# Kernel optimization log

Hardware: AMD Instinct MI355X
Metric: run time of the kernel (lower is better)

Reference implementation:

```python
import jax, jax.numpy as jnp
import numpy as np

N_NODES = 100000
N_EDGES = 1600000
F_IN = 512
HEADS = 8
C1 = 8            # hidden per head in conv1
N_CLASSES = 40
NEG_SLOPE = 0.2
EPS = 1e-16


def setup_inputs() -> dict:
    key = jax.random.key(0)
    ks = jax.random.split(key, 12)
    x = jax.random.normal(ks[0], (N_NODES, F_IN), dtype=jnp.float32)
    # edges with src != dst (PyG SuperGAT removes then re-adds self-loops)
    src = jax.random.randint(ks[1], (N_EDGES,), 0, N_NODES)
    off = jax.random.randint(ks[2], (N_EDGES,), 1, N_NODES)
    dst = (src + off) % N_NODES
    edge_index = jnp.stack([src, dst]).astype(jnp.int64)
    def glorot(k, shape):
        fan = shape[0] + shape[-1]
        return jax.random.uniform(k, shape, jnp.float32, -1.0, 1.0) * np.sqrt(6.0 / fan)
    W1 = glorot(ks[3], (F_IN, HEADS * C1))
    att_l1 = glorot(ks[4], (HEADS, C1))
    att_r1 = glorot(ks[5], (HEADS, C1))
    b1 = jnp.zeros((HEADS * C1,), jnp.float32)
    W2 = glorot(ks[6], (HEADS * C1, HEADS * N_CLASSES))
    att_l2 = glorot(ks[7], (HEADS, N_CLASSES))
    att_r2 = glorot(ks[8], (HEADS, N_CLASSES))
    b2 = jnp.zeros((N_CLASSES,), jnp.float32)
    return {"x": x, "edge_index": edge_index, "W1": W1, "att_l1": att_l1,
            "att_r1": att_r1, "b1": b1, "W2": W2, "att_l2": att_l2,
            "att_r2": att_r2, "b2": b2}


def supergat_conv(x, edge_index, W, att_l, att_r, bias, concat):
    """SuperGATConv with attention_type='MX', eval mode (no dropout)."""
    N = x.shape[0]
    H, C = att_l.shape
    xw = (x @ W).reshape(N, H, C)
    loops = jnp.arange(N)
    src = jnp.concatenate([edge_index[0], loops])  # j (source)
    dst = jnp.concatenate([edge_index[1], loops])  # i (target)
    x_j = xw[src]                                   # [E,H,C]
    x_i = xw[dst]                                   # [E,H,C]
    # MX attention: GO score gated by sigmoid of DP logits
    logits = jnp.einsum('ehc,ehc->eh', x_i, x_j)
    alpha = jnp.einsum('ehc,hc->eh', x_j, att_l) + jnp.einsum('ehc,hc->eh', x_i, att_r)
    alpha = alpha * jax.nn.sigmoid(logits)
    alpha = jax.nn.leaky_relu(alpha, NEG_SLOPE)
    # segment softmax over incoming edges of each destination node
    amax = jax.ops.segment_max(alpha, dst, num_segments=N)
    e = jnp.exp(alpha - amax[dst])
    denom = jax.ops.segment_sum(e, dst, num_segments=N)
    a = e / (denom[dst] + EPS)
    out = jax.ops.segment_sum(x_j * a[..., None], dst, num_segments=N)  # [N,H,C]
    out = out.reshape(N, H * C) if concat else out.mean(axis=1)
    return out + bias


def reference(x, edge_index, W1, att_l1, att_r1, b1, W2, att_l2, att_r2, b2):
    # eval mode: F.dropout(p=0.6) is identity, att_loss is 0
    h = jax.nn.elu(supergat_conv(x, edge_index, W1, att_l1, att_r1, b1, concat=True))
    out = supergat_conv(h, edge_index, W2, att_l2, att_r2, b2, concat=False)
    att_loss = jnp.float32(0.0)
    return jax.nn.log_softmax(out, axis=-1), att_loss
```

## Files before the change

### kernel.cpp

```cpp
#include <hip/hip_runtime.h>
#include <cstdint>

#define N_NODES 100000
#define N_EDGES 1600000
#define SCAN_NB 196

typedef short bf16x8 __attribute__((ext_vector_type(8)));
typedef float f32x4 __attribute__((ext_vector_type(4)));
typedef float f32x2 __attribute__((ext_vector_type(2)));

__device__ __forceinline__ uint16_t f2bf(float f) {
    uint32_t b = __float_as_uint(f);
    return (uint16_t)((b + 0x7fffu + ((b >> 16) & 1u)) >> 16);
}
__device__ __forceinline__ float bfval(uint16_t u) {
    return __uint_as_float(((uint32_t)u) << 16);
}
__device__ __forceinline__ float blo(uint32_t u) { return __uint_as_float(u << 16); }
__device__ __forceinline__ float bhi(uint32_t u) { return __uint_as_float(u & 0xffff0000u); }

__device__ __forceinline__ float fast_rcp(float x) { return __builtin_amdgcn_rcpf(x); }
__device__ __forceinline__ float swz_xadd8(float x) {
    int s = __builtin_amdgcn_ds_swizzle(__float_as_int(x), 0x201F);
    return x + __int_as_float(s);
}
__device__ __forceinline__ float swz_xadd16(float x) {
    int s = __builtin_amdgcn_ds_swizzle(__float_as_int(x), 0x401F);
    return x + __int_as_float(s);
}

__global__ __launch_bounds__(512) void prep_k(const float* __restrict__ W1,
        const float* __restrict__ W2, const float* __restrict__ attl,
        const float* __restrict__ attr,
        uint16_t* __restrict__ w1hi, uint16_t* __restrict__ w1lo,
        float* __restrict__ wl2, float* __restrict__ wr2,
        uint16_t* __restrict__ w2z, uint16_t* __restrict__ mhi,
        uint16_t* __restrict__ mlo) {
    __shared__ float Wh[64 * 40];
    int b = blockIdx.x, tid = threadIdx.x;
    if (b < 8) {
        int gid = b * 512 + tid;
        int c = gid & 63, kg = gid >> 6;
        uint32_t dh[4], dl[4];
        #pragma unroll
        for (int t = 0; t < 4; ++t) {
            float v0 = W1[(kg * 8 + 2 * t) * 64 + c];
            float v1 = W1[(kg * 8 + 2 * t + 1) * 64 + c];
            uint16_t h0 = f2bf(v0), h1 = f2bf(v1);
            uint16_t l0 = f2bf(v0 - bfval(h0)), l1 = f2bf(v1 - bfval(h1));
            dh[t] = h0 | ((uint32_t)h1 << 16);
            dl[t] = l0 | ((uint32_t)l1 << 16);
        }
        *(uint4*)(w1hi + (long)c * 512 + kg * 8) = make_uint4(dh[0], dh[1], dh[2], dh[3]);
        *(uint4*)(w1lo + (long)c * 512 + kg * 8) = make_uint4(dl[0], dl[1], dl[2], dl[3]);
    } else if (b == 8) {
        int h = tid >> 6, k = tid & 63;
        float sl = 0.f, sr = 0.f;
        #pragma unroll 8
        for (int c = 0; c < 40; ++c) {
            float w = W2[k * 320 + h * 40 + c];
            sl += w * attl[h * 40 + c];
            sr += w * attr[h * 40 + c];
        }
        wl2[tid] = sl; wr2[tid] = sr;
    } else if (b < 57) {
        int t = (b - 9) * 512 + tid;
        int c = t >> 9, kap = t & 511;
        int h = kap >> 6, k = kap & 63;
        float v = (c < 40) ? W2[k * 320 + h * 40 + c] : 0.f;
        w2z[c * 512 + kap] = f2bf(v);
    } else {
        int h = b - 57;
        for (int t = tid; t < 2560; t += 512) {
            int k = t / 40, c = t % 40;
            Wh[k * 40 + c] = W2[k * 320 + h * 40 + c];
        }
        __syncthreads();
        #pragma unroll
        for (int r = 0; r < 8; ++r) {
            int o = r * 512 + tid;
            int kp = o >> 6, k = o & 63;
            float s = 0.f;
            #pragma unroll 8
            for (int c = 0; c < 40; ++c) s += Wh[k * 40 + c] * Wh[kp * 40 + c];
            uint16_t hi = f2bf(s);
            uint16_t lo = f2bf(s - bfval(hi));
            mhi[(h * 64 + kp) * 64 + k] = hi;
            mlo[(h * 64 + kp) * 64 + k] = lo;
        }
    }
}

__global__ __launch_bounds__(512) void gemm1_mfma(const float* __restrict__ x,
        const uint16_t* __restrict__ w1hi, const uint16_t* __restrict__ w1lo,
        float* __restrict__ xw1, uint16_t* __restrict__ xw1b) {
    __shared__ __align__(16) char Ah[128 * 144];
    __shared__ __align__(16) char Al[128 * 144];
    __shared__ __align__(16) char Bh[64 * 144];
    __shared__ __align__(16) char Bl[64 * 144];
    int tid = threadIdx.x;
    int l = tid & 63, w = tid >> 6;
    long base = (long)blockIdx.x * 128;
    f32x4 acc[4];
    #pragma unroll
    for (int ct = 0; ct < 4; ++ct)
        #pragma unroll
        for (int j = 0; j < 4; ++j) acc[ct][j] = 0.f;

    for (int kb = 0; kb < 512; kb += 64) {
        __syncthreads();
        #pragma unroll
        for (int it = 0; it < 2; ++it) {
            int idx = tid + it * 512;
            int row = idx >> 3, kc = idx & 7;
            long r = base + row; if (r >= N_NODES) r = N_NODES - 1;
            const float4* p = (const float4*)(x + r * 512 + kb + kc * 8);
            float4 f0 = p[0], f1 = p[1];
            float v[8] = {f0.x, f0.y, f0.z, f0.w, f1.x, f1.y, f1.z, f1.w};
            uint32_t dh[4], dl[4];
            #pragma unroll
            for (int t = 0; t < 4; ++t) {
                uint16_t h0 = f2bf(v[2 * t]),     h1 = f2bf(v[2 * t + 1]);
                uint16_t l0 = f2bf(v[2 * t] - bfval(h0));
                uint16_t l1 = f2bf(v[2 * t + 1] - bfval(h1));
                dh[t] = h0 | ((uint32_t)h1 << 16);
                dl[t] = l0 | ((uint32_t)l1 << 16);
            }
            *(uint4*)(Ah + row * 144 + kc * 16) = make_uint4(dh[0], dh[1], dh[2], dh[3]);
            *(uint4*)(Al + row * 144 + kc * 16) = make_uint4(dl[0], dl[1], dl[2], dl[3]);
        }
        {
            int c = tid >> 3, kc = tid & 7;
            *(uint4*)(Bh + c * 144 + kc * 16) =
                *(const uint4*)(w1hi + (long)c * 512 + kb + kc * 8);
            *(uint4*)(Bl + c * 144 + kc * 16) =
                *(const uint4*)(w1lo + (long)c * 512 + kb + kc * 8);
        }
        __syncthreads();
        #pragma unroll
        for (int kk = 0; kk < 2; ++kk) {
            int aoff = (w * 16 + (l & 15)) * 144 + kk * 64 + (l >> 4) * 16;
            bf16x8 ah = *(const bf16x8*)(Ah + aoff);
            bf16x8 alo = *(const bf16x8*)(Al + aoff);
            #pragma unroll
            for (int ct = 0; ct < 4; ++ct) {
                int boff = (ct * 16 + (l & 15)) * 144 + kk * 64 + (l >> 4) * 16;
                bf16x8 bh = *(const bf16x8*)(Bh + boff);
                bf16x8 bl = *(const bf16x8*)(Bl + boff);
                acc[ct] = __builtin_amdgcn_mfma_f32_16x16x32_bf16(ah, bh, acc[ct], 0, 0, 0);
                acc[ct] = __builtin_amdgcn_mfma_f32_16x16x32_bf16(alo, bh, acc[ct], 0, 0, 0);
                acc[ct] = __builtin_amdgcn_mfma_f32_16x16x32_bf16(ah, bl, acc[ct], 0, 0, 0);
            }
        }
    }
    int nrow = w * 16 + (l >> 4) * 4;
    #pragma unroll
    for (int ct = 0; ct < 4; ++ct)
        #pragma unroll
        for (int j = 0; j < 4; ++j) {
            long node = base + nrow + j;
            if (node < N_NODES) {
                int col = ct * 16 + (l & 15);
                xw1[node * 64 + col] = acc[ct][j];
                xw1b[node * 64 + col] = f2bf(acc[ct][j]);
            }
        }
}

__global__ __launch_bounds__(512) void ygemm_mfma(const uint16_t* __restrict__ hjb,
        const uint16_t* __restrict__ mhi, const uint16_t* __restrict__ mlo,
        uint16_t* __restrict__ Y16) {
    __shared__ __align__(16) char Bh[256 * 144];
    __shared__ __align__(16) char Bl[256 * 144];
    int tid = threadIdx.x;
    int l = tid & 63, w = tid >> 6;
    int half = blockIdx.x & 1;
    long base = (long)(blockIdx.x >> 1) * 128;
    #pragma unroll
    for (int it = 0; it < 4; ++it) {
        int idx = tid + it * 512;
        int c = idx >> 3, kc = idx & 7;
        *(uint4*)(Bh + c * 144 + kc * 16) =
            *(const uint4*)(mhi + (long)(half * 256 + c) * 64 + kc * 8);
        *(uint4*)(Bl + c * 144 + kc * 16) =
            *(const uint4*)(mlo + (long)(half * 256 + c) * 64 + kc * 8);
    }
    long n0 = base + w * 16 + (l & 15);
    long nld = n0 < N_NODES ? n0 : N_NODES - 1;
    bf16x8 a[2];
    #pragma unroll
    for (int kk = 0; kk < 2; ++kk)
        a[kk] = *(const bf16x8*)(hjb + nld * 64 + kk * 32 + (l >> 4) * 8);
    __syncthreads();
    f32x4 acc[16];
    #pragma unroll
    for (int ct = 0; ct < 16; ++ct)
        #pragma unroll
        for (int j = 0; j < 4; ++j) acc[ct][j] = 0.f;
    #pragma unroll
    for (int ct = 0; ct < 16; ++ct) {
        #pragma unroll
        for (int kk = 0; kk < 2; ++kk) {
            bf16x8 bh = *(const bf16x8*)(Bh + (ct * 16 + (l & 15)) * 144 + kk * 64 + (l >> 4) * 16);
            bf16x8 bl = *(const bf16x8*)(Bl + (ct * 16 + (l & 15)) * 144 + kk * 64 + (l >> 4) * 16);
            acc[ct] = __builtin_amdgcn_mfma_f32_16x16x32_bf16(bh, a[kk], acc[ct], 0, 0, 0);
            acc[ct] = __builtin_amdgcn_mfma_f32_16x16x32_bf16(bl, a[kk], acc[ct], 0, 0, 0);
        }
    }
    if (n0 < N_NODES) {
        uint32_t* Yd = (uint32_t*)Y16;
        #pragma unroll
        for (int ct = 0; ct < 16; ++ct) {
            int kp = half * 256 + ct * 16 + (l >> 4) * 4;
            uint32_t d0 = f2bf(acc[ct][0]) | ((uint32_t)f2bf(acc[ct][1]) << 16);
            uint32_t d1 = f2bf(acc[ct][2]) | ((uint32_t)f2bf(acc[ct][3]) << 16);
            Yd[n0 * 256 + (kp >> 1)]     = d0;
            Yd[n0 * 256 + (kp >> 1) + 1] = d1;
        }
    }
}

__global__ void hist_k(const int* __restrict__ dst, int* __restrict__ deg) {
    int e = blockIdx.x * blockDim.x + threadIdx.x;
    if (e < N_EDGES) atomicAdd(&deg[dst[e]], 1);
}

__global__ __launch_bounds__(512) void scan_a(const int* __restrict__ deg,
        int* __restrict__ offs, int* __restrict__ btot) {
    __shared__ int sh[512];
    int t = threadIdx.x;
    int g = blockIdx.x * 512 + t;
    int v = (g < N_NODES) ? deg[g] : 0;
    sh[t] = v;
    __syncthreads();
    #pragma unroll
    for (int o = 1; o < 512; o <<= 1) {
        int add = (t >= o) ? sh[t - o] : 0;
        __syncthreads();
        sh[t] += add;
        __syncthreads();
    }
    if (g < N_NODES) offs[g] = sh[t] - v;
    if (t == 511) btot[blockIdx.x] = sh[511];
}

__global__ __launch_bounds__(256) void scan_b(int* __restrict__ btot) {
    __shared__ int sh[256];
    int t = threadIdx.x;
    int v = (t < SCAN_NB) ? btot[t] : 0;
    sh[t] = v;
    __syncthreads();
    #pragma unroll
    for (int o = 1; o < 256; o <<= 1) {
        int add = (t >= o) ? sh[t - o] : 0;
        __syncthreads();
        sh[t] += add;
        __syncthreads();
    }
    if (t < SCAN_NB) btot[t] = sh[t] - v;
}

__global__ __launch_bounds__(512) void scan_c(int* __restrict__ offs,
        const int* __restrict__ btot, int* __restrict__ cursor) {
    int g = blockIdx.x * 512 + threadIdx.x;
    if (g < N_NODES) {
        int o = offs[g] + btot[blockIdx.x];
        offs[g] = o;
        cursor[g] = o;
    }
}

__global__ void scatter_k(const int* __restrict__ src, const int* __restrict__ dst,
        int* __restrict__ cursor, int* __restrict__ csr8) {
    int e = blockIdx.x * blockDim.x + threadIdx.x;
    if (e < N_EDGES) {
        int pos = atomicAdd(&cursor[dst[e]], 1);
        csr8[pos] = src[e] << 3;
    }
}

__global__ __launch_bounds__(256) void conv1_node(const float* __restrict__ xw,
        const uint16_t* __restrict__ xwb,
        const int* __restrict__ offs, const int* __restrict__ deg,
        const int* __restrict__ csr8, const float* __restrict__ att_l,
        const float* __restrict__ att_r, const float* __restrict__ b1,
        const float* __restrict__ wl2, const float* __restrict__ wr2,
        uint16_t* __restrict__ hjb, float* __restrict__ al, float* __restrict__ ar) {
    int wid = (blockIdx.x * blockDim.x + threadIdx.x) >> 6;
    if (wid >= N_NODES) return;
    int i = wid;
    int lane = threadIdx.x & 63;
    int g = lane >> 3, h = lane & 7;
    const float4* rowi = (const float4*)(xw + (long)i * 64 + h * 8);
    float4 xi0 = rowi[0], xi1 = rowi[1];
    f32x2 xip[4] = {{xi0.x, xi0.y}, {xi0.z, xi0.w}, {xi1.x, xi1.y}, {xi1.z, xi1.w}};
    const float4* alp4 = (const float4*)(att_l + h * 8);
    float4 t0 = alp4[0], t1 = alp4[1];
    f32x2 atlp[4] = {{t0.x, t0.y}, {t0.z, t0.w}, {t1.x, t1.y}, {t1.z, t1.w}};
    const float4* arp4 = (const float4*)(att_r + h * 8);
    float4 u0 = arp4[0], u1 = arp4[1];
    f32x2 atrp[4] = {{u0.x, u0.y}, {u0.z, u0.w}, {u1.x, u1.y}, {u1.z, u1.w}};
    f32x2 prp = xip[0] * atrp[0];
    prp += xip[1] * atrp[1];
    prp += xip[2] * atrp[2];
    prp += xip[3] * atrp[3];
    float pr = prp.x + prp.y;
    f32x2 accp[4] = {{0.f,0.f},{0.f,0.f},{0.f,0.f},{0.f,0.f}};
    float den = 0.f;

#define C1_EDGE(XJP) do { \
    f32x2 qdp = xip[0] * (XJP)[0]; \
    qdp += xip[1] * (XJP)[1]; \
    qdp += xip[2] * (XJP)[2]; \
    qdp += xip[3] * (XJP)[3]; \
    f32x2 qlp = (XJP)[0] * atlp[0]; \
    qlp += (XJP)[1] * atlp[1]; \
    qlp += (XJP)[2] * atlp[2]; \
    qlp += (XJP)[3] * atlp[3]; \
    float qd = qdp.x + qdp.y, ql = qlp.x + qlp.y; \
    float a = (ql + pr) * fast_rcp(1.0f + __expf(-qd)); \
    a = fmaxf(a, 0.2f * a); \
    float e = __expf(a); \
    den += e; \
    f32x2 ev = {e, e}; \
    accp[0] += ev * (XJP)[0]; \
    accp[1] += ev * (XJP)[1]; \
    accp[2] += ev * (XJP)[2]; \
    accp[3] += ev * (XJP)[3]; \
} while (0)

    if (g == 0) C1_EDGE(xip);
    int off = offs[i], dg = deg[i];
    int k = g;
    for (; k + 8 < dg; k += 16) {
        int j0 = csr8[off + k], j1 = csr8[off + k + 8];
        uint4 q0 = *(const uint4*)(xwb + (long)j0 * 8 + h * 8);
        uint4 q1 = *(const uint4*)(xwb + (long)j1 * 8 + h * 8);
        f32x2 ap[4] = {{blo(q0.x), bhi(q0.x)}, {blo(q0.y), bhi(q0.y)},
                       {blo(q0.z), bhi(q0.z)}, {blo(q0.w), bhi(q0.w)}};
        f32x2 bp[4] = {{blo(q1.x), bhi(q1.x)}, {blo(q1.y), bhi(q1.y)},
                       {blo(q1.z), bhi(q1.z)}, {blo(q1.w), bhi(q1.w)}};
        C1_EDGE(ap);
        C1_EDGE(bp);
    }
    if (k < dg) {
        int j0 = csr8[off + k];
        uint4 q0 = *(const uint4*)(xwb + (long)j0 * 8 + h * 8);
        f32x2 ap[4] = {{blo(q0.x), bhi(q0.x)}, {blo(q0.y), bhi(q0.y)},
                       {blo(q0.z), bhi(q0.z)}, {blo(q0.w), bhi(q0.w)}};
        C1_EDGE(ap);
    }
#undef C1_EDGE

    float acc[8] = {accp[0].x, accp[0].y, accp[1].x, accp[1].y,
                    accp[2].x, accp[2].y, accp[3].x, accp[3].y};
    #pragma unroll
    for (int o = 8; o <= 32; o <<= 1) {
        #pragma unroll
        for (int t = 0; t < 8; ++t) acc[t] += __shfl_xor(acc[t], o);
        den += __shfl_xor(den, o);
    }
    float inv = fast_rcp(den + 1e-16f);
    const float4* bp4 = (const float4*)(b1 + h * 8);
    float4 c0 = bp4[0], c1 = bp4[1];
    float bias[8] = {c0.x, c0.y, c0.z, c0.w, c1.x, c1.y, c1.z, c1.w};
    float ov[8];
    #pragma unroll
    for (int t = 0; t < 8; ++t) {
        float v = acc[t] * inv + bias[t];
        ov[t] = v > 0.f ? v : __expf(v) - 1.0f;
    }
    if (g == 0) {
        uint32_t d0 = f2bf(ov[0]) | ((uint32_t)f2bf(ov[1]) << 16);
        uint32_t d1 = f2bf(ov[2]) | ((uint32_t)f2bf(ov[3]) << 16);
        uint32_t d2 = f2bf(ov[4]) | ((uint32_t)f2bf(ov[5]) << 16);
        uint32_t d3 = f2bf(ov[6]) | ((uint32_t)f2bf(ov[7]) << 16);
        *(uint4*)(hjb + (long)i * 64 + h * 8) = make_uint4(d0, d1, d2, d3);
    }
    {
        const float4* wlp = (const float4*)(wl2 + g * 64 + h * 8);
        float4 w0 = wlp[0], w1 = wlp[1];
        const float4* wrp = (const float4*)(wr2 + g * 64 + h * 8);
        float4 r0 = wrp[0], r1 = wrp[1];
        float sl = ov[0]*w0.x + ov[1]*w0.y + ov[2]*w0.z + ov[3]*w0.w
                 + ov[4]*w1.x + ov[5]*w1.y + ov[6]*w1.z + ov[7]*w1.w;
        float sr = ov[0]*r0.x + ov[1]*r0.y + ov[2]*r0.z + ov[3]*r0.w
                 + ov[4]*r1.x + ov[5]*r1.y + ov[6]*r1.z + ov[7]*r1.w;
        #pragma unroll
        for (int o = 1; o <= 4; o <<= 1) {
            sl += __shfl_xor(sl, o);
            sr += __shfl_xor(sr, o);
        }
        if (h == 0) {
            al[i * 8 + g] = sl;
            ar[i * 8 + g] = sr;
        }
    }
}

__global__ __launch_bounds__(256) void conv2_node(const uint16_t* __restrict__ hjb16,
        const int* __restrict__ offs, const int* __restrict__ deg,
        const int* __restrict__ csr8, const float* __restrict__ al,
        const float* __restrict__ ar, uint32_t* __restrict__ Yd) {
    int wid = (blockIdx.x * 256 + threadIdx.x) >> 6;
    if (wid >= N_NODES) return;
    int i = wid;
    int lane = threadIdx.x & 63;
    int half = lane >> 5;
    int lam = lane & 7, r2 = (lane >> 3) & 3;
    const uint4* hj4 = (const uint4*)hjb16;
    int r22 = r2 * 2;
    unsigned ydw = (unsigned)i * 256u + (unsigned)lam * 32u + (unsigned)r2 * 8u;

    f32x2 y[8];
    {
        uint4 a = *(const uint4*)(Yd + ydw);
        uint4 b = *(const uint4*)(Yd + ydw + 4);
        uint32_t d[8] = {a.x, a.y, a.z, a.w, b.x, b.y, b.z, b.w};
        #pragma unroll
        for (int t = 0; t < 8; ++t) y[t] = (f32x2){blo(d[t]), bhi(d[t])};
    }
    float ari = ar[i * 8 + lam];
    f32x2 agg[8];
    #pragma unroll
    for (int t = 0; t < 8; ++t) agg[t] = (f32x2){0.f, 0.f};
    float den = 0.f;
    int off = offs[i], dg = deg[i];

    auto CORE = [&](const uint32_t* D, float alv) {
        f32x2 h[8];
        #pragma unroll
        for (int t = 0; t < 8; ++t) h[t] = (f32x2){blo(D[t]), bhi(D[t])};
        f32x2 pp = y[0] * h[0];
        #pragma unroll
        for (int t = 1; t < 8; ++t) pp += y[t] * h[t];
        float pd = pp.x + pp.y;
        pd = swz_xadd8(pd);
        pd = swz_xadd16(pd);
        float a = (alv + ari) * fast_rcp(1.0f + __expf(-pd));
        a = fmaxf(a, 0.2f * a);
        float e = __expf(a);
        den += e;
        f32x2 ev = {e, e};
        #pragma unroll
        for (int t = 0; t < 8; ++t) agg[t] += ev * h[t];
    };
    auto COREG = [&](const uint32_t* D, float alv, bool valid) {
        f32x2 h[8];
        #pragma unroll
        for (int t = 0; t < 8; ++t) h[t] = (f32x2){blo(D[t]), bhi(D[t])};
        f32x2 pp = y[0] * h[0];
        #pragma unroll
        for (int t = 1; t < 8; ++t) pp += y[t] * h[t];
        float pd = pp.x + pp.y;
        pd = swz_xadd8(pd);
        pd = swz_xadd16(pd);
        float a = (alv + ari) * fast_rcp(1.0f + __expf(-pd));
        a = fmaxf(a, 0.2f * a);
        float e = __expf(a);
        e = valid ? e : 0.f;
        den += e;
        f32x2 ev = {e, e};
        #pragma unroll
        for (int t = 0; t < 8; ++t) agg[t] += ev * h[t];
    };
    auto PF = [&](int p, uint32_t* D, float& A) {
        p = p < N_EDGES ? p : N_EDGES - 1;
        int j = csr8[p];
        const uint4* r = hj4 + (unsigned)j + r22;
        uint4 a = r[0], b = r[1];
        D[0] = a.x; D[1] = a.y; D[2] = a.z; D[3] = a.w;
        D[4] = b.x; D[5] = b.y; D[6] = b.z; D[7] = b.w;
        A = al[j + lam];
    };

    {
        uint32_t DS[8]; float AS;
        const uint4* r = hj4 + (unsigned)i * 8u + r22;
        uint4 a = r[0], b = r[1];
        DS[0] = a.x; DS[1] = a.y; DS[2] = a.z; DS[3] = a.w;
        DS[4] = b.x; DS[5] = b.y; DS[6] = b.z; DS[7] = b.w;
        AS = al[i * 8 + lam];
        COREG(DS, AS, half == 0);
    }

    int nP = dg >> 1;
    int base = off + half;
    uint32_t R0[8], R1[8], T0[8], T1[8];
    float A0, A1, B0, B1;
    PF(base,     R0, A0);
    PF(base + 2, R1, A1);
    int s = 0;
    while (s + 4 <= nP) {
        PF(base + 2*s + 4,  T0, B0); CORE(R0, A0);
        PF(base + 2*s + 6,  T1, B1); CORE(R1, A1);
        PF(base + 2*s + 8,  R0, A0); CORE(T0, B0);
        PF(base + 2*s + 10, R1, A1); CORE(T1, B1);
        s += 4;
    }
    int rem = nP - s;
    if (rem >= 2) {
        PF(base + 2*s + 4, T0, B0);
        CORE(R0, A0);
        CORE(R1, A1);
        if (rem == 3) CORE(T0, B0);
    } else if (rem == 1) {
        CORE(R0, A0);
    }
    if (dg & 1) {
        uint32_t RT[8]; float AT;
        PF(off + dg - 1, RT, AT);
        COREG(RT, AT, half == 0);
    }

    den += __shfl_xor(den, 32);
    #pragma unroll
    for (int t = 0; t < 8; ++t) {
        agg[t].x += __shfl_xor(agg[t].x, 32);
        agg[t].y += __shfl_xor(agg[t].y, 32);
    }
    float inv = 0.125f * fast_rcp(den + 1e-16f);
    if (half == 0) {
        uint32_t zd[8];
        #pragma unroll
        for (int t = 0; t < 8; ++t) {
            float zx = agg[t].x * inv, zy = agg[t].y * inv;
            zd[t] = f2bf(zx) | ((uint32_t)f2bf(zy) << 16);
        }
        *(uint4*)(Yd + ydw)     = make_uint4(zd[0], zd[1], zd[2], zd[3]);
        *(uint4*)(Yd + ydw + 4) = make_uint4(zd[4], zd[5], zd[6], zd[7]);
    }
}

__global__ __launch_bounds__(512) void zgemm_mfma(const uint32_t* __restrict__ Zd,
        const uint16_t* __restrict__ w2z, const float* __restrict__ b2,
        float* __restrict__ out) {
    __shared__ __align__(16) uint16_t Bsm[48 * 520];
    int tid = threadIdx.x;
    int l = tid & 63, w = tid >> 6;
    long base = (long)blockIdx.x * 128;
    for (int q = tid; q < 3072; q += 512) {
        int c = q >> 6, k8 = (q & 63) * 8;
        *(uint4*)(Bsm + c * 520 + k8) = *(const uint4*)(w2z + c * 512 + k8);
    }
    if (blockIdx.x == 0 && tid == 0) out[(long)N_NODES * 40] = 0.0f;
    __syncthreads();
    long n0 = base + w * 16 + (l & 15);
    long nld = n0 < N_NODES ? n0 : N_NODES - 1;
    f32x4 acc[3];
    #pragma unroll
    for (int ct = 0; ct < 3; ++ct)
        #pragma unroll
        for (int j = 0; j < 4; ++j) acc[ct][j] = 0.f;
    #pragma unroll
    for (int kb = 0; kb < 16; ++kb) {
        bf16x8 a = *(const bf16x8*)(Zd + nld * 256 + kb * 16 + (l >> 4) * 4);
        #pragma unroll
        for (int ct = 0; ct < 3; ++ct) {
            bf16x8 b = *(const bf16x8*)(Bsm + (ct * 16 + (l & 15)) * 520 + kb * 32 + (l >> 4) * 8);
            acc[ct] = __builtin_amdgcn_mfma_f32_16x16x32_bf16(b, a, acc[ct], 0, 0, 0);
        }
    }
    float v[12];
    int cb0 = (l >> 4) * 4;
    #pragma unroll
    for (int ct = 0; ct < 3; ++ct)
        #pragma unroll
        for (int j = 0; j < 4; ++j) {
            int cb = ct * 16 + cb0 + j;
            v[ct * 4 + j] = (cb < 40) ? acc[ct][j] + b2[cb] : -1e30f;
        }
    float mx = v[0];
    #pragma unroll
    for (int t = 1; t < 12; ++t) mx = fmaxf(mx, v[t]);
    mx = fmaxf(mx, __shfl_xor(mx, 16));
    mx = fmaxf(mx, __shfl_xor(mx, 32));
    float sm = 0.f;
    #pragma unroll
    for (int t = 0; t < 12; ++t) sm += (v[t] > -1e29f) ? __expf(v[t] - mx) : 0.f;
    sm += __shfl_xor(sm, 16);
    sm += __shfl_xor(sm, 32);
    float lse = mx + __logf(sm);
    if (n0 < N_NODES) {
        #pragma unroll
        for (int ct = 0; ct < 3; ++ct)
            #pragma unroll
            for (int j = 0; j < 4; ++j) {
                int cb = ct * 16 + cb0 + j;
                if (cb < 40) out[n0 * 40 + cb] = v[ct * 4 + j] - lse;
            }
    }
}

extern "C" void kernel_launch(void* const* d_in, const int* in_sizes, int n_in,
                              void* d_out, int out_size, void* d_ws, size_t ws_size,
                              hipStream_t stream) {
    const float* x      = (const float*)d_in[0];
    const int*   ei     = (const int*)d_in[1];
    const float* W1     = (const float*)d_in[2];
    const float* att_l1 = (const float*)d_in[3];
    const float* att_r1 = (const float*)d_in[4];
    const float* b1     = (const float*)d_in[5];
    const float* W2     = (const float*)d_in[6];
    const float* att_l2 = (const float*)d_in[7];
    const float* att_r2 = (const float*)d_in[8];
    const float* b2     = (const float*)d_in[9];
    const int* src = ei;
    const int* dst = ei + N_EDGES;
    float* out = (float*)d_out;

    char* ws = (char*)d_ws;
    uint16_t* Y      = (uint16_t*)(ws + 0);
    float*    xw1    = (float*)(ws + 0);
    uint16_t* xw1b   = (uint16_t*)(ws + 25600000);
    uint16_t* hjb    = (uint16_t*)(ws + 102400000);
    float*    al     = (float*)(ws + 115200000);
    float*    ar     = (float*)(ws + 118400000);
    int*      deg    = (int*)(ws + 121600000);
    int*      offs   = (int*)(ws + 122000000);
    int*      cursor = (int*)(ws + 122400000);
    int*      btot   = (int*)(ws + 122800000);
    int*      csr8   = (int*)(ws + 122801024);
    uint16_t* w1hi   = (uint16_t*)(ws + 129201024);
    uint16_t* w1lo   = (uint16_t*)(ws + 129266560);
    uint16_t* mhi    = (uint16_t*)(ws + 129332096);
    uint16_t* mlo    = (uint16_t*)(ws + 129397632);
    uint16_t* w2z    = (uint16_t*)(ws + 129463168);
    float*    wl2    = (float*)(ws + 129512320);
    float*    wr2    = (float*)(ws + 129514368);

    hipMemsetAsync(deg, 0, (size_t)N_NODES * 4, stream);

    prep_k<<<65, 512, 0, stream>>>(W1, W2, att_l2, att_r2,
                                   w1hi, w1lo, wl2, wr2, w2z, mhi, mlo);

    hist_k<<<6250, 256, 0, stream>>>(dst, deg);
    scan_a<<<SCAN_NB, 512, 0, stream>>>(deg, offs, btot);
    scan_b<<<1, 256, 0, stream>>>(btot);
    scan_c<<<SCAN_NB, 512, 0, stream>>>(offs, btot, cursor);
    scatter_k<<<6250, 256, 0, stream>>>(src, dst, cursor, csr8);

    gemm1_mfma<<<782, 512, 0, stream>>>(x, w1hi, w1lo, xw1, xw1b);
    conv1_node<<<25000, 256, 0, stream>>>(xw1, xw1b, offs, deg, csr8,
                                          att_l1, att_r1, b1, wl2, wr2,
                                          hjb, al, ar);

    ygemm_mfma<<<1564, 512, 0, stream>>>(hjb, mhi, mlo, Y);

    conv2_node<<<25000, 256, 0, stream>>>(hjb, offs, deg, csr8, al, ar, (uint32_t*)Y);

    zgemm_mfma<<<782, 512, 0, stream>>>((const uint32_t*)Y, w2z, b2, out);
}
```

Measured before the change: 561.6 us.

## Software-pipeline index and row loads in both GAT aggregation loops

Both aggregation kernels now use a three-stage rotating pipeline. Neighbor indices are loaded two steps ahead and neighbor rows one step ahead, which decouples the dependent index-then-row load chain so more gather latency overlaps with compute. The conv1 loop switches from a 2-edge unrolled loop with a tail to masked triple buffering, so some iterations do wasted masked work and clamped over-fetches. Holding more rows in flight also raises register pressure.

```diff
diff --git a/kernel.cpp b/kernel.cpp
--- a/kernel.cpp
+++ b/kernel.cpp
@@ -307,50 +307,60 @@
     float pr = prp.x + prp.y;
     f32x2 accp[4] = {{0.f,0.f},{0.f,0.f},{0.f,0.f},{0.f,0.f}};
     float den = 0.f;
-
-#define C1_EDGE(XJP) do { \
-    f32x2 qdp = xip[0] * (XJP)[0]; \
-    qdp += xip[1] * (XJP)[1]; \
-    qdp += xip[2] * (XJP)[2]; \
-    qdp += xip[3] * (XJP)[3]; \
-    f32x2 qlp = (XJP)[0] * atlp[0]; \
-    qlp += (XJP)[1] * atlp[1]; \
-    qlp += (XJP)[2] * atlp[2]; \
-    qlp += (XJP)[3] * atlp[3]; \
-    float qd = qdp.x + qdp.y, ql = qlp.x + qlp.y; \
-    float a = (ql + pr) * fast_rcp(1.0f + __expf(-qd)); \
-    a = fmaxf(a, 0.2f * a); \
-    float e = __expf(a); \
-    den += e; \
-    f32x2 ev = {e, e}; \
-    accp[0] += ev * (XJP)[0]; \
-    accp[1] += ev * (XJP)[1]; \
-    accp[2] += ev * (XJP)[2]; \
-    accp[3] += ev * (XJP)[3]; \
-} while (0)
-
-    if (g == 0) C1_EDGE(xip);
     int off = offs[i], dg = deg[i];
-    int k = g;
-    for (; k + 8 < dg; k += 16) {
-        int j0 = csr8[off + k], j1 = csr8[off + k + 8];
-        uint4 q0 = *(const uint4*)(xwb + (long)j0 * 8 + h * 8);
-        uint4 q1 = *(const uint4*)(xwb + (long)j1 * 8 + h * 8);
-        f32x2 ap[4] = {{blo(q0.x), bhi(q0.x)}, {blo(q0.y), bhi(q0.y)},
-                       {blo(q0.z), bhi(q0.z)}, {blo(q0.w), bhi(q0.w)}};
-        f32x2 bp[4] = {{blo(q1.x), bhi(q1.x)}, {blo(q1.y), bhi(q1.y)},
-                       {blo(q1.z), bhi(q1.z)}, {blo(q1.w), bhi(q1.w)}};
-        C1_EDGE(ap);
-        C1_EDGE(bp);
-    }
-    if (k < dg) {
-        int j0 = csr8[off + k];
-        uint4 q0 = *(const uint4*)(xwb + (long)j0 * 8 + h * 8);
-        f32x2 ap[4] = {{blo(q0.x), bhi(q0.x)}, {blo(q0.y), bhi(q0.y)},
-                       {blo(q0.z), bhi(q0.z)}, {blo(q0.w), bhi(q0.w)}};
-        C1_EDGE(ap);
-    }
-#undef C1_EDGE
+
+    auto CORE1 = [&](const f32x2* xjp, bool valid) {
+        f32x2 qdp = xip[0] * xjp[0];
+        qdp += xip[1] * xjp[1];
+        qdp += xip[2] * xjp[2];
+        qdp += xip[3] * xjp[3];
+        f32x2 qlp = xjp[0] * atlp[0];
+        qlp += xjp[1] * atlp[1];
+        qlp += xjp[2] * atlp[2];
+        qlp += xjp[3] * atlp[3];
+        float qd = qdp.x + qdp.y, ql = qlp.x + qlp.y;
+        float a = (ql + pr) * fast_rcp(1.0f + __expf(-qd));
+        a = fmaxf(a, 0.2f * a);
+        float e = __expf(a);
+        e = valid ? e : 0.f;
+        den += e;
+        f32x2 ev = {e, e};
+        accp[0] += ev * xjp[0];
+        accp[1] += ev * xjp[1];
+        accp[2] += ev * xjp[2];
+        accp[3] += ev * xjp[3];
+    };
+    auto C1Q = [&](uint4 q, bool valid) {
+        f32x2 ap[4] = {{blo(q.x), bhi(q.x)}, {blo(q.y), bhi(q.y)},
+                       {blo(q.z), bhi(q.z)}, {blo(q.w), bhi(q.w)}};
+        CORE1(ap, valid);
+    };
+    auto LI = [&](int S) -> int {
+        int p = off + g + 8 * S;
+        p = p < N_EDGES ? p : N_EDGES - 1;
+        return csr8[p];
+    };
+    auto RW = [&](uint4& q, int j) {
+        q = *(const uint4*)(xwb + (long)j * 8 + h * 8);
+    };
+
+    CORE1(xip, g == 0);
+
+    int nS = (dg + 7) >> 3;
+    int jA = LI(0), jB = LI(1), jC = LI(2);
+    uint4 qA, qB, qC;
+    RW(qA, jA); jA = LI(3);
+    RW(qB, jB); jB = LI(4);
+    RW(qC, jC); jC = LI(5);
+    int S = 0;
+    while (S + 3 <= nS) {
+        C1Q(qA, g + 8 * S < dg);       RW(qA, jA); jA = LI(S + 6);
+        C1Q(qB, g + 8 * (S + 1) < dg); RW(qB, jB); jB = LI(S + 7);
+        C1Q(qC, g + 8 * (S + 2) < dg); RW(qC, jC); jC = LI(S + 8);
+        S += 3;
+    }
+    if (S < nS)     C1Q(qA, g + 8 * S < dg);
+    if (S + 1 < nS) C1Q(qB, g + 8 * (S + 1) < dg);
 
     float acc[8] = {accp[0].x, accp[0].y, accp[1].x, accp[1].y,
                     accp[2].x, accp[2].y, accp[3].x, accp[3].y};
@@ -464,9 +474,11 @@
         #pragma unroll
         for (int t = 0; t < 8; ++t) agg[t] += ev * h[t];
     };
-    auto PF = [&](int p, uint32_t* D, float& A) {
+    auto LIDX = [&](int p) -> int {
         p = p < N_EDGES ? p : N_EDGES - 1;
-        int j = csr8[p];
+        return csr8[p];
+    };
+    auto ROW = [&](uint32_t* D, float& A, int j) {
         const uint4* r = hj4 + (unsigned)j + r22;
         uint4 a = r[0], b = r[1];
         D[0] = a.x; D[1] = a.y; D[2] = a.z; D[3] = a.w;
@@ -476,40 +488,31 @@
 
     {
         uint32_t DS[8]; float AS;
-        const uint4* r = hj4 + (unsigned)i * 8u + r22;
-        uint4 a = r[0], b = r[1];
-        DS[0] = a.x; DS[1] = a.y; DS[2] = a.z; DS[3] = a.w;
-        DS[4] = b.x; DS[5] = b.y; DS[6] = b.z; DS[7] = b.w;
-        AS = al[i * 8 + lam];
+        ROW(DS, AS, i * 8);
         COREG(DS, AS, half == 0);
     }
 
     int nP = dg >> 1;
     int base = off + half;
-    uint32_t R0[8], R1[8], T0[8], T1[8];
-    float A0, A1, B0, B1;
-    PF(base,     R0, A0);
-    PF(base + 2, R1, A1);
+    uint32_t RA[8], RB[8], RC[8];
+    float AA, AB, AC;
+    int jA = LIDX(base), jB = LIDX(base + 2), jC = LIDX(base + 4);
+    ROW(RA, AA, jA); jA = LIDX(base + 6);
+    ROW(RB, AB, jB); jB = LIDX(base + 8);
+    ROW(RC, AC, jC); jC = LIDX(base + 10);
     int s = 0;
-    while (s + 4 <= nP) {
-        PF(base + 2*s + 4,  T0, B0); CORE(R0, A0);
-        PF(base + 2*s + 6,  T1, B1); CORE(R1, A1);
-        PF(base + 2*s + 8,  R0, A0); CORE(T0, B0);
-        PF(base + 2*s + 10, R1, A1); CORE(T1, B1);
-        s += 4;
+    while (s + 3 <= nP) {
+        CORE(RA, AA); ROW(RA, AA, jA); jA = LIDX(base + 2 * s + 12);
+        CORE(RB, AB); ROW(RB, AB, jB); jB = LIDX(base + 2 * s + 14);
+        CORE(RC, AC); ROW(RC, AC, jC); jC = LIDX(base + 2 * s + 16);
+        s += 3;
     }
     int rem = nP - s;
-    if (rem >= 2) {
-        PF(base + 2*s + 4, T0, B0);
-        CORE(R0, A0);
-        CORE(R1, A1);
-        if (rem == 3) CORE(T0, B0);
-    } else if (rem == 1) {
-        CORE(R0, A0);
-    }
+    if (rem >= 1) CORE(RA, AA);
+    if (rem >= 2) CORE(RB, AB);
     if (dg & 1) {
         uint32_t RT[8]; float AT;
-        PF(off + dg - 1, RT, AT);
+        ROW(RT, AT, LIDX(off + dg - 1));
         COREG(RT, AT, half == 0);
     }
 
```

Result: slower. 590.6 us (+5.2%).
